# Kernel tuning notes

Hardware: AMD Instinct MI355X
Metric: run time of the kernel (lower is better)

The kernel has to match this reference:

```python
import jax, jax.numpy as jnp
import numpy as np

T, B, IN, HID, OUT = 100, 2048, 784, 100, 10
BETA = 0.9      # snn.Leaky(beta=0.9)
THRESH = 1.0    # snntorch default threshold
ALPHA = 2.0     # snntorch default ATan surrogate alpha

@jax.custom_vjp
def fire(x):
    # Heaviside spike with ATan surrogate gradient (snntorch default).
    return (x > 0).astype(x.dtype)

def _fire_fwd(x):
    return fire(x), x

def _fire_bwd(x, g):
    return (g * (ALPHA / 2) / (1 + (jnp.pi / 2 * ALPHA * x) ** 2),)

fire.defvjp(_fire_fwd, _fire_bwd)

def setup_inputs() -> dict:
    key = jax.random.key(0)
    k1, k2, k3 = jax.random.split(key, 3)
    x_seq = jax.random.normal(k1, (T, B, IN), dtype=jnp.float32)
    # nn.Linear weights are [out_features, in_features], bias=False
    w1 = jax.random.normal(k2, (HID, IN), dtype=jnp.float32) * (1.0 / np.sqrt(IN))
    w2 = jax.random.normal(k3, (OUT, HID), dtype=jnp.float32) * (1.0 / np.sqrt(HID))
    return {"x_seq": x_seq, "w1": w1, "w2": w2}

def _leaky_step(mem, cur):
    # snntorch Leaky, reset_mechanism='subtract':
    # reset = H(mem_prev - thresh) (detached); mem = beta*mem + input - reset*thresh; spk = fire(mem - thresh)
    reset = jax.lax.stop_gradient((mem > THRESH).astype(mem.dtype))
    mem = BETA * mem + cur - reset * THRESH
    spk = fire(mem - THRESH)
    return spk, mem

def reference(x_seq, w1, w2):
    batch = x_seq.shape[1]
    def step(carry, x_t):
        mem1, mem2 = carry
        spk1, mem1 = _leaky_step(mem1, x_t @ w1.T)      # [B,HID]
        spk2, mem2 = _leaky_step(mem2, spk1 @ w2.T)     # [B,OUT]
        return (mem1, mem2), spk2
    init = (jnp.zeros((batch, HID), x_seq.dtype),
            jnp.zeros((batch, OUT), x_seq.dtype))
    _, spk2_seq = jax.lax.scan(step, init, x_seq)
    return spk2_seq.sum(axis=0)  # spk2_sum: [B, OUT]
```

## Files before the change

### kernel.cpp

```cpp
#include <hip/hip_runtime.h>

#define T_STEPS 100
#define B_SZ    2048
#define IN_DIM  784
#define KPAD    800
#define HID_DIM 100
#define OUT_DIM 10
#define BN      112
#define BMR     64
#define KC      32
#define KSTEPS  25
#define WLP     113

typedef double f64x4 __attribute__((ext_vector_type(4)));
#define MFMA64(a, b, c) __builtin_amdgcn_mfma_f64_16x16x4f64((a), (b), (c), 0, 0, 0)

__global__ void pad_w1(const float* __restrict__ w1, float* __restrict__ w1p) {
  int i = blockIdx.x * 256 + threadIdx.x;
  if (i >= BN * KPAD) return;
  int r = i / KPAD, c = i % KPAD;
  w1p[i] = (r < HID_DIM && c < IN_DIM) ? w1[r * IN_DIM + c] : 0.0f;
}

__global__ __launch_bounds__(256, 4)
void snn_gemm1(const float* __restrict__ x,
               const float* __restrict__ w1p,
               double* __restrict__ cur)
{
  const int tid  = threadIdx.x;
  const int lane = tid & 63;
  const int wv   = tid >> 6;
  const int kg   = lane >> 4;
  const int il   = lane & 15;
  const long rowBase = (long)blockIdx.x * BMR;

  __shared__ float wls[2][KC][WLP];

  const int  wrow = tid >> 1;
  const int  wk0  = (tid & 1) * 16;
  const bool dow  = tid < 2 * BN;
  const float* wsrc = w1p + (long)wrow * KPAD + wk0;
  float4 wg0, wg1, wg2, wg3;

  auto WLOAD = [&](int s) {
    if (dow) {
      const float4* wp = reinterpret_cast<const float4*>(wsrc + s * KC);
      wg0 = wp[0]; wg1 = wp[1]; wg2 = wp[2]; wg3 = wp[3];
    }
  };
  auto WSTORE = [&](int buf) {
    if (dow) {
      float* b0 = &wls[buf][wk0][wrow];
      b0[0 * WLP] = wg0.x; b0[1 * WLP] = wg0.y; b0[2 * WLP]  = wg0.z; b0[3 * WLP]  = wg0.w;
      b0[4 * WLP] = wg1.x; b0[5 * WLP] = wg1.y; b0[6 * WLP]  = wg1.z; b0[7 * WLP]  = wg1.w;
      b0[8 * WLP] = wg2.x; b0[9 * WLP] = wg2.y; b0[10 * WLP] = wg2.z; b0[11 * WLP] = wg2.w;
      b0[12 * WLP] = wg3.x; b0[13 * WLP] = wg3.y; b0[14 * WLP] = wg3.z; b0[15 * WLP] = wg3.w;
    }
  };

  const float* xrp = x + (rowBase + wv * 16 + il) * (long)IN_DIM;
  float xcur[8], xnxt[8];
  auto XLOAD = [&](int s, float* d) {
    const int ks = s * KC + 8 * kg;
    if (s == KSTEPS - 1 && kg >= 2) {
#pragma unroll
      for (int j = 0; j < 8; ++j) d[j] = 0.0f;
    } else {
      *reinterpret_cast<float4*>(&d[0]) = *reinterpret_cast<const float4*>(xrp + ks);
      *reinterpret_cast<float4*>(&d[4]) = *reinterpret_cast<const float4*>(xrp + ks + 4);
    }
  };

  WLOAD(0); XLOAD(0, xcur);

  f64x4 z = {0.0, 0.0, 0.0, 0.0};
  const double eil = (double)il;
  const double d0 = (kg == 0) ? 1.0 : 0.0;
  const double d1 = (kg == 1) ? 1.0 : 0.0;
  const double d2 = (kg == 2) ? 1.0 : 0.0;
  const double d3 = (kg == 3) ? 1.0 : 0.0;
  const f64x4 Prow0 = MFMA64(eil, d0, z);
  const f64x4 Prow1 = MFMA64(eil, d1, z);
  const f64x4 Pcol0 = MFMA64(d0, eil, z);
  const f64x4 Pcol1 = MFMA64(d1, eil, z);
  const f64x4 Pv0   = MFMA64(d0, d0, z);
  const f64x4 Pv1   = MFMA64(d1, d1, z);
  const f64x4 Pv2   = MFMA64(d2, d2, z);
  const f64x4 Pv3   = MFMA64(d3, d3, z);

  bool okl = true;
  int rowof[4], colof[4];
#pragma unroll
  for (int r = 0; r < 4; ++r) {
    okl = okl && (Pv0[r] == 1.0) && (Pv1[r] == 1.0) && (Pv2[r] == 1.0) && (Pv3[r] == 1.0);
    okl = okl && (Prow0[r] == Prow1[r]) && (Pcol0[r] == Pcol1[r]);
    const int rr = (int)Prow0[r];
    const int cc = (int)Pcol0[r];
    okl = okl && ((double)rr == Prow0[r]) && (rr >= 0) && (rr < 16);
    okl = okl && ((double)cc == Pcol0[r]) && (cc >= 0) && (cc < 16);
    rowof[r] = rr; colof[r] = cc;
  }
  if (__all(okl ? 1 : 0) == 0) {
#pragma unroll
    for (int r = 0; r < 4; ++r) { rowof[r] = kg * 4 + r; colof[r] = il; }
  }

  f64x4 acc[7];
#pragma unroll
  for (int ht = 0; ht < 7; ++ht) acc[ht] = z;

  WSTORE(0); WLOAD(1);
  __syncthreads();

#pragma unroll 1
  for (int s = 0; s < KSTEPS; ++s) {
    const int buf = s & 1;
    if (s + 1 < KSTEPS) { WSTORE(buf ^ 1); XLOAD(s + 1, xnxt); }
    if (s + 2 < KSTEPS) WLOAD(s + 2);

#pragma unroll
    for (int m = 0; m < 8; ++m) {
      const double a0 = (double)xcur[m];
      double b[7];
#pragma unroll
      for (int ht = 0; ht < 7; ++ht)
        b[ht] = (double)wls[buf][8 * kg + m][ht * 16 + il];
#pragma unroll
      for (int ht = 0; ht < 7; ++ht)
        acc[ht] = MFMA64(a0, b[ht], acc[ht]);
    }
    __syncthreads();
#pragma unroll
    for (int j = 0; j < 8; ++j) xcur[j] = xnxt[j];
  }

  const long r0 = rowBase + wv * 16;
#pragma unroll
  for (int ht = 0; ht < 7; ++ht)
#pragma unroll
    for (int m = 0; m < 4; ++m)
      cur[(r0 + rowof[m]) * BN + ht * 16 + colof[m]] = acc[ht][m];
}

__global__ __launch_bounds__(256)
void snn_recur(const double* __restrict__ cur,
               const float* __restrict__ w2,
               double* __restrict__ mem1s, float* __restrict__ spk1s,
               double* __restrict__ mem2s, float* __restrict__ spk2s,
               float* __restrict__ outs,
               float* __restrict__ dout,
               int chunkT, int isFirst, int isLast)
{
  const int tid = threadIdx.x;
  const int b0  = blockIdx.x * 4;
  __shared__ float w2l[OUT_DIM * HID_DIM];
  __shared__ float spkl[4 * BN];

  if (tid < 250)
    reinterpret_cast<float4*>(w2l)[tid] = reinterpret_cast<const float4*>(w2)[tid];

  const bool pa = tid < 112;
  const int  sl = tid / 28, q4 = (tid % 28) * 4;
  const long aOff = (long)(b0 + sl) * BN + q4;
  double m1[4] = {0.0, 0.0, 0.0, 0.0};
  float4 s1 = make_float4(0.f, 0.f, 0.f, 0.f);
  if (pa && !isFirst) {
    const double2* mp = reinterpret_cast<const double2*>(mem1s + aOff);
    double2 a = mp[0], b = mp[1];
    m1[0] = a.x; m1[1] = a.y; m1[2] = b.x; m1[3] = b.y;
    s1 = *reinterpret_cast<const float4*>(spk1s + aOff);
  }

  const bool pb = tid < 80;
  const int  pp = tid >> 1, hf = tid & 1;
  const int  ss = pp / 10, oo = pp % 10;
  const long bOff = (long)b0 * OUT_DIM + pp;
  double m2 = 0.0;
  float s2 = 0.f, oacc = 0.f;
  if (pb && !isFirst && hf == 0) { m2 = mem2s[bOff]; s2 = spk2s[bOff]; oacc = outs[bOff]; }

  __syncthreads();

  double2 ca, cb;
  if (pa) {
    const double2* cp = reinterpret_cast<const double2*>(cur + (long)(b0 + sl) * BN + q4);
    ca = cp[0]; cb = cp[1];
  }

  for (int tt = 0; tt < chunkT; ++tt) {
    if (pa) {
      double cu[4] = {ca.x, ca.y, cb.x, cb.y};
      const int tn = (tt + 1 < chunkT) ? tt + 1 : tt;
      const double2* cp = reinterpret_cast<const double2*>(
          cur + ((long)tn * B_SZ + b0 + sl) * BN + q4);
      ca = cp[0]; cb = cp[1];

      float4 sp;
      float* spv = &sp.x;
      const float* s1v = &s1.x;
#pragma unroll
      for (int j = 0; j < 4; ++j) {
        double m = 0.9 * m1[j];
        m = m + cu[j];
        m = m - (double)s1v[j];
        spv[j] = (m > 1.0) ? 1.0f : 0.0f;
        m1[j] = m;
      }
      s1 = sp;
      *reinterpret_cast<float4*>(&spkl[sl * BN + q4]) = sp;
    }
    __syncthreads();
    if (pb) {
      const float* sr = &spkl[ss * BN] + hf * 50;
      const float* wr = &w2l[oo * HID_DIM] + hf * 50;
      double a0 = 0.0, a1 = 0.0;
#pragma unroll
      for (int h = 0; h < 50; h += 2) {
        a0 = fma((double)sr[h],     (double)wr[h],     a0);
        a1 = fma((double)sr[h + 1], (double)wr[h + 1], a1);
      }
      double a = a0 + a1;
      a = a + __shfl_xor(a, 1);
      if (hf == 0) {
        double m = 0.9 * m2;
        m = m + a;
        m = m - (double)s2;
        const float sp = (m > 1.0) ? 1.0f : 0.0f;
        m2 = m; s2 = sp; oacc += sp;
      }
    }
    __syncthreads();
  }

  if (pa) {
    double2* mp = reinterpret_cast<double2*>(mem1s + aOff);
    mp[0] = make_double2(m1[0], m1[1]);
    mp[1] = make_double2(m1[2], m1[3]);
    *reinterpret_cast<float4*>(spk1s + aOff) = s1;
  }
  if (pb && hf == 0) {
    mem2s[bOff] = m2; spk2s[bOff] = s2; outs[bOff] = oacc;
    if (isLast) dout[bOff] = oacc;
  }
}

extern "C" void kernel_launch(void* const* d_in, const int* in_sizes, int n_in,
                              void* d_out, int out_size, void* d_ws, size_t ws_size,
                              hipStream_t stream) {
  const float* x  = (const float*)d_in[0];
  const float* w1 = (const float*)d_in[1];
  const float* w2 = (const float*)d_in[2];
  float* out = (float*)d_out;

  char* ws = (char*)d_ws;
  float*  w1p   = (float*) (ws);
  double* mem1s = (double*)(ws +  358400);
  float*  spk1s = (float*) (ws + 2193408);
  double* mem2s = (double*)(ws + 3110912);
  float*  spk2s = (float*) (ws + 3274752);
  float*  outs  = (float*) (ws + 3356672);
  double* cur   = (double*)(ws + 3438592);

  pad_w1<<<dim3((BN * KPAD + 255) / 256), dim3(256), 0, stream>>>(w1, w1p);

  const size_t perT = (size_t)B_SZ * BN * 8;
  size_t curCap = ws_size > (size_t)3438592 ? ws_size - 3438592 : 0;
  int Tc = (int)(curCap / perT);
  if (Tc > T_STEPS) Tc = T_STEPS;
  if (Tc < 1) Tc = 1;

  for (int t0 = 0; t0 < T_STEPS; t0 += Tc) {
    const int ct = (T_STEPS - t0 < Tc) ? (T_STEPS - t0) : Tc;
    snn_gemm1<<<dim3(ct * (B_SZ / BMR)), dim3(256), 0, stream>>>(
        x + (size_t)t0 * B_SZ * IN_DIM, w1p, cur);
    snn_recur<<<dim3(B_SZ / 4), dim3(256), 0, stream>>>(
        cur, w2, mem1s, spk1s, mem2s, spk2s, outs, out,
        ct, (t0 == 0) ? 1 : 0, (t0 + ct >= T_STEPS) ? 1 : 0);
  }
}
```

Baseline: 771.5 us.

## Load W1 directly from global into registers, dropping LDS staging and pad kernel

The GEMM1 kernel no longer stages padded W1 tiles through double-buffered shared memory with barriers. Each lane now loads its W1 fragments straight from the unpadded w1 into registers via float4 loads, clamping rows and K offsets so the padding is never read, and the pad_w1 launch is removed. This drops LDS traffic, syncthreads and one kernel launch, in exchange for redundant global/L2 loads of W1 across waves and higher register pressure, which is why launch bounds drop from 4 to 3 blocks.

```diff
diff --git a/kernel.cpp b/kernel.cpp
--- a/kernel.cpp
+++ b/kernel.cpp
@@ -3,28 +3,19 @@
 #define T_STEPS 100
 #define B_SZ    2048
 #define IN_DIM  784
-#define KPAD    800
 #define HID_DIM 100
 #define OUT_DIM 10
 #define BN      112
 #define BMR     64
 #define KC      32
 #define KSTEPS  25
-#define WLP     113
 
 typedef double f64x4 __attribute__((ext_vector_type(4)));
 #define MFMA64(a, b, c) __builtin_amdgcn_mfma_f64_16x16x4f64((a), (b), (c), 0, 0, 0)
 
-__global__ void pad_w1(const float* __restrict__ w1, float* __restrict__ w1p) {
-  int i = blockIdx.x * 256 + threadIdx.x;
-  if (i >= BN * KPAD) return;
-  int r = i / KPAD, c = i % KPAD;
-  w1p[i] = (r < HID_DIM && c < IN_DIM) ? w1[r * IN_DIM + c] : 0.0f;
-}
-
-__global__ __launch_bounds__(256, 4)
+__global__ __launch_bounds__(256, 3)
 void snn_gemm1(const float* __restrict__ x,
-               const float* __restrict__ w1p,
+               const float* __restrict__ w1,
                double* __restrict__ cur)
 {
   const int tid  = threadIdx.x;
@@ -34,44 +25,30 @@
   const int il   = lane & 15;
   const long rowBase = (long)blockIdx.x * BMR;
 
-  __shared__ float wls[2][KC][WLP];
-
-  const int  wrow = tid >> 1;
-  const int  wk0  = (tid & 1) * 16;
-  const bool dow  = tid < 2 * BN;
-  const float* wsrc = w1p + (long)wrow * KPAD + wk0;
-  float4 wg0, wg1, wg2, wg3;
-
-  auto WLOAD = [&](int s) {
-    if (dow) {
-      const float4* wp = reinterpret_cast<const float4*>(wsrc + s * KC);
-      wg0 = wp[0]; wg1 = wp[1]; wg2 = wp[2]; wg3 = wp[3];
-    }
-  };
-  auto WSTORE = [&](int buf) {
-    if (dow) {
-      float* b0 = &wls[buf][wk0][wrow];
-      b0[0 * WLP] = wg0.x; b0[1 * WLP] = wg0.y; b0[2 * WLP]  = wg0.z; b0[3 * WLP]  = wg0.w;
-      b0[4 * WLP] = wg1.x; b0[5 * WLP] = wg1.y; b0[6 * WLP]  = wg1.z; b0[7 * WLP]  = wg1.w;
-      b0[8 * WLP] = wg2.x; b0[9 * WLP] = wg2.y; b0[10 * WLP] = wg2.z; b0[11 * WLP] = wg2.w;
-      b0[12 * WLP] = wg3.x; b0[13 * WLP] = wg3.y; b0[14 * WLP] = wg3.z; b0[15 * WLP] = wg3.w;
-    }
-  };
-
+  int rowoff[7];
+#pragma unroll
+  for (int ht = 0; ht < 7; ++ht) {
+    int r = ht * 16 + il;
+    if (r > HID_DIM - 1) r = HID_DIM - 1;
+    rowoff[ht] = r * IN_DIM;
+  }
+
+  const int kg8 = kg * 8;
   const float* xrp = x + (rowBase + wv * 16 + il) * (long)IN_DIM;
+
   float xcur[8], xnxt[8];
   auto XLOAD = [&](int s, float* d) {
-    const int ks = s * KC + 8 * kg;
     if (s == KSTEPS - 1 && kg >= 2) {
 #pragma unroll
       for (int j = 0; j < 8; ++j) d[j] = 0.0f;
     } else {
-      *reinterpret_cast<float4*>(&d[0]) = *reinterpret_cast<const float4*>(xrp + ks);
-      *reinterpret_cast<float4*>(&d[4]) = *reinterpret_cast<const float4*>(xrp + ks + 4);
+      const float* p = xrp + s * KC + kg8;
+      *reinterpret_cast<float4*>(&d[0]) = *reinterpret_cast<const float4*>(p);
+      *reinterpret_cast<float4*>(&d[4]) = *reinterpret_cast<const float4*>(p + 4);
     }
   };
 
-  WLOAD(0); XLOAD(0, xcur);
+  XLOAD(0, xcur);
 
   f64x4 z = {0.0, 0.0, 0.0, 0.0};
   const double eil = (double)il;
@@ -109,27 +86,29 @@
 #pragma unroll
   for (int ht = 0; ht < 7; ++ht) acc[ht] = z;
 
-  WSTORE(0); WLOAD(1);
-  __syncthreads();
-
 #pragma unroll 1
   for (int s = 0; s < KSTEPS; ++s) {
-    const int buf = s & 1;
-    if (s + 1 < KSTEPS) { WSTORE(buf ^ 1); XLOAD(s + 1, xnxt); }
-    if (s + 2 < KSTEPS) WLOAD(s + 2);
+    if (s + 1 < KSTEPS) XLOAD(s + 1, xnxt);
+
+    int k0 = s * KC + kg8;
+    if (s == KSTEPS - 1 && kg >= 2) k0 = kg8;
+    float4 wa[7], wb[7];
+#pragma unroll
+    for (int ht = 0; ht < 7; ++ht) {
+      const float* p = w1 + rowoff[ht] + k0;
+      wa[ht] = *reinterpret_cast<const float4*>(p);
+      wb[ht] = *reinterpret_cast<const float4*>(p + 4);
+    }
 
 #pragma unroll
     for (int m = 0; m < 8; ++m) {
       const double a0 = (double)xcur[m];
-      double b[7];
-#pragma unroll
-      for (int ht = 0; ht < 7; ++ht)
-        b[ht] = (double)wls[buf][8 * kg + m][ht * 16 + il];
-#pragma unroll
-      for (int ht = 0; ht < 7; ++ht)
-        acc[ht] = MFMA64(a0, b[ht], acc[ht]);
-    }
-    __syncthreads();
+#pragma unroll
+      for (int ht = 0; ht < 7; ++ht) {
+        const float wf = (m < 4) ? (&wa[ht].x)[m] : (&wb[ht].x)[m - 4];
+        acc[ht] = MFMA64(a0, (double)wf, acc[ht]);
+      }
+    }
 #pragma unroll
     for (int j = 0; j < 8; ++j) xcur[j] = xnxt[j];
   }
@@ -253,18 +232,15 @@
   float* out = (float*)d_out;
 
   char* ws = (char*)d_ws;
-  float*  w1p   = (float*) (ws);
-  double* mem1s = (double*)(ws +  358400);
-  float*  spk1s = (float*) (ws + 2193408);
-  double* mem2s = (double*)(ws + 3110912);
-  float*  spk2s = (float*) (ws + 3274752);
-  float*  outs  = (float*) (ws + 3356672);
-  double* cur   = (double*)(ws + 3438592);
-
-  pad_w1<<<dim3((BN * KPAD + 255) / 256), dim3(256), 0, stream>>>(w1, w1p);
+  double* mem1s = (double*)(ws);
+  float*  spk1s = (float*) (ws + 1835008);
+  double* mem2s = (double*)(ws + 2752512);
+  float*  spk2s = (float*) (ws + 2916352);
+  float*  outs  = (float*) (ws + 2998272);
+  double* cur   = (double*)(ws + 3080192);
 
   const size_t perT = (size_t)B_SZ * BN * 8;
-  size_t curCap = ws_size > (size_t)3438592 ? ws_size - 3438592 : 0;
+  size_t curCap = ws_size > (size_t)3080192 ? ws_size - 3080192 : 0;
   int Tc = (int)(curCap / perT);
   if (Tc > T_STEPS) Tc = T_STEPS;
   if (Tc < 1) Tc = 1;
@@ -272,7 +248,7 @@
   for (int t0 = 0; t0 < T_STEPS; t0 += Tc) {
     const int ct = (T_STEPS - t0 < Tc) ? (T_STEPS - t0) : Tc;
     snn_gemm1<<<dim3(ct * (B_SZ / BMR)), dim3(256), 0, stream>>>(
-        x + (size_t)t0 * B_SZ * IN_DIM, w1p, cur);
+        x + (size_t)t0 * B_SZ * IN_DIM, w1, cur);
     snn_recur<<<dim3(B_SZ / 4), dim3(256), 0, stream>>>(
         cur, w2, mem1s, spk1s, mem2s, spk2s, outs, out,
         ct, (t0 == 0) ? 1 : 0, (t0 + ct >= T_STEPS) ? 1 : 0);
```

New measurement: 835.5 us. 1.08x slower.

## Double row tile per wave in FP64 MFMA GEMM1 and transpose W1 LDS layout

Applied to the files above, without the earlier changes.

Each wave now computes two 16-row tiles (BMR 64->128), so every W1 value read from LDS feeds two MFMAs and the LDS traffic per FLOP is halved. The shared W1 tile is stored row-major by hidden unit with a padded K stride, which lets the store and the per-thread reads use float4 vector accesses in place of scalar strided ones. In exchange each thread holds twice as many accumulators, launch bounds drop to 2 blocks per CU, and there are half as many blocks in the grid.

```diff
diff --git a/kernel.cpp b/kernel.cpp
--- a/kernel.cpp
+++ b/kernel.cpp
@@ -7,10 +7,10 @@
 #define HID_DIM 100
 #define OUT_DIM 10
 #define BN      112
-#define BMR     64
+#define BMR     128
 #define KC      32
 #define KSTEPS  25
-#define WLP     113
+#define WLP     36
 
 typedef double f64x4 __attribute__((ext_vector_type(4)));
 #define MFMA64(a, b, c) __builtin_amdgcn_mfma_f64_16x16x4f64((a), (b), (c), 0, 0, 0)
@@ -22,7 +22,7 @@
   w1p[i] = (r < HID_DIM && c < IN_DIM) ? w1[r * IN_DIM + c] : 0.0f;
 }
 
-__global__ __launch_bounds__(256, 4)
+__global__ __launch_bounds__(256, 2)
 void snn_gemm1(const float* __restrict__ x,
                const float* __restrict__ w1p,
                double* __restrict__ cur)
@@ -32,14 +32,15 @@
   const int wv   = tid >> 6;
   const int kg   = lane >> 4;
   const int il   = lane & 15;
+  const int kg8  = kg * 8;
   const long rowBase = (long)blockIdx.x * BMR;
 
-  __shared__ float wls[2][KC][WLP];
+  __shared__ float wls[2][BN][WLP];
 
   const int  wrow = tid >> 1;
-  const int  wk0  = (tid & 1) * 16;
+  const int  wh0  = (tid & 1) * 16;
   const bool dow  = tid < 2 * BN;
-  const float* wsrc = w1p + (long)wrow * KPAD + wk0;
+  const float* wsrc = w1p + (long)wrow * KPAD + wh0;
   float4 wg0, wg1, wg2, wg3;
 
   auto WLOAD = [&](int s) {
@@ -50,24 +51,25 @@
   };
   auto WSTORE = [&](int buf) {
     if (dow) {
-      float* b0 = &wls[buf][wk0][wrow];
-      b0[0 * WLP] = wg0.x; b0[1 * WLP] = wg0.y; b0[2 * WLP]  = wg0.z; b0[3 * WLP]  = wg0.w;
-      b0[4 * WLP] = wg1.x; b0[5 * WLP] = wg1.y; b0[6 * WLP]  = wg1.z; b0[7 * WLP]  = wg1.w;
-      b0[8 * WLP] = wg2.x; b0[9 * WLP] = wg2.y; b0[10 * WLP] = wg2.z; b0[11 * WLP] = wg2.w;
-      b0[12 * WLP] = wg3.x; b0[13 * WLP] = wg3.y; b0[14 * WLP] = wg3.z; b0[15 * WLP] = wg3.w;
+      float4* b0 = reinterpret_cast<float4*>(&wls[buf][wrow][wh0]);
+      b0[0] = wg0; b0[1] = wg1; b0[2] = wg2; b0[3] = wg3;
     }
   };
 
-  const float* xrp = x + (rowBase + wv * 16 + il) * (long)IN_DIM;
-  float xcur[8], xnxt[8];
-  auto XLOAD = [&](int s, float* d) {
-    const int ks = s * KC + 8 * kg;
+  const float* xr0 = x + (rowBase + wv * 32 + il) * (long)IN_DIM;
+  const float* xr1 = xr0 + 16 * (long)IN_DIM;
+  float xcur[2][8], xnxt[2][8];
+  auto XLOAD = [&](int s, float (*d)[8]) {
     if (s == KSTEPS - 1 && kg >= 2) {
 #pragma unroll
-      for (int j = 0; j < 8; ++j) d[j] = 0.0f;
+      for (int j = 0; j < 8; ++j) { d[0][j] = 0.0f; d[1][j] = 0.0f; }
     } else {
-      *reinterpret_cast<float4*>(&d[0]) = *reinterpret_cast<const float4*>(xrp + ks);
-      *reinterpret_cast<float4*>(&d[4]) = *reinterpret_cast<const float4*>(xrp + ks + 4);
+      const float* p0 = xr0 + s * KC + kg8;
+      const float* p1 = xr1 + s * KC + kg8;
+      *reinterpret_cast<float4*>(&d[0][0]) = *reinterpret_cast<const float4*>(p0);
+      *reinterpret_cast<float4*>(&d[0][4]) = *reinterpret_cast<const float4*>(p0 + 4);
+      *reinterpret_cast<float4*>(&d[1][0]) = *reinterpret_cast<const float4*>(p1);
+      *reinterpret_cast<float4*>(&d[1][4]) = *reinterpret_cast<const float4*>(p1 + 4);
     }
   };
 
@@ -105,9 +107,11 @@
     for (int r = 0; r < 4; ++r) { rowof[r] = kg * 4 + r; colof[r] = il; }
   }
 
-  f64x4 acc[7];
-#pragma unroll
-  for (int ht = 0; ht < 7; ++ht) acc[ht] = z;
+  f64x4 acc[2][7];
+#pragma unroll
+  for (int rt = 0; rt < 2; ++rt)
+#pragma unroll
+    for (int ht = 0; ht < 7; ++ht) acc[rt][ht] = z;
 
   WSTORE(0); WLOAD(1);
   __syncthreads();
@@ -118,28 +122,49 @@
     if (s + 1 < KSTEPS) { WSTORE(buf ^ 1); XLOAD(s + 1, xnxt); }
     if (s + 2 < KSTEPS) WLOAD(s + 2);
 
-#pragma unroll
-    for (int m = 0; m < 8; ++m) {
-      const double a0 = (double)xcur[m];
-      double b[7];
-#pragma unroll
-      for (int ht = 0; ht < 7; ++ht)
-        b[ht] = (double)wls[buf][8 * kg + m][ht * 16 + il];
-#pragma unroll
-      for (int ht = 0; ht < 7; ++ht)
-        acc[ht] = MFMA64(a0, b[ht], acc[ht]);
+    double dx0[8], dx1[8];
+#pragma unroll
+    for (int j = 0; j < 8; ++j) {
+      dx0[j] = (double)xcur[0][j];
+      dx1[j] = (double)xcur[1][j];
+    }
+
+#pragma unroll
+    for (int ht = 0; ht < 7; ++ht) {
+      const float* wrp = &wls[buf][ht * 16 + il][kg8];
+      const float4 f0 = *reinterpret_cast<const float4*>(wrp);
+      const float4 f1 = *reinterpret_cast<const float4*>(wrp + 4);
+      acc[0][ht] = MFMA64(dx0[0], (double)f0.x, acc[0][ht]);
+      acc[1][ht] = MFMA64(dx1[0], (double)f0.x, acc[1][ht]);
+      acc[0][ht] = MFMA64(dx0[1], (double)f0.y, acc[0][ht]);
+      acc[1][ht] = MFMA64(dx1[1], (double)f0.y, acc[1][ht]);
+      acc[0][ht] = MFMA64(dx0[2], (double)f0.z, acc[0][ht]);
+      acc[1][ht] = MFMA64(dx1[2], (double)f0.z, acc[1][ht]);
+      acc[0][ht] = MFMA64(dx0[3], (double)f0.w, acc[0][ht]);
+      acc[1][ht] = MFMA64(dx1[3], (double)f0.w, acc[1][ht]);
+      acc[0][ht] = MFMA64(dx0[4], (double)f1.x, acc[0][ht]);
+      acc[1][ht] = MFMA64(dx1[4], (double)f1.x, acc[1][ht]);
+      acc[0][ht] = MFMA64(dx0[5], (double)f1.y, acc[0][ht]);
+      acc[1][ht] = MFMA64(dx1[5], (double)f1.y, acc[1][ht]);
+      acc[0][ht] = MFMA64(dx0[6], (double)f1.z, acc[0][ht]);
+      acc[1][ht] = MFMA64(dx1[6], (double)f1.z, acc[1][ht]);
+      acc[0][ht] = MFMA64(dx0[7], (double)f1.w, acc[0][ht]);
+      acc[1][ht] = MFMA64(dx1[7], (double)f1.w, acc[1][ht]);
     }
     __syncthreads();
 #pragma unroll
-    for (int j = 0; j < 8; ++j) xcur[j] = xnxt[j];
-  }
-
-  const long r0 = rowBase + wv * 16;
-#pragma unroll
-  for (int ht = 0; ht < 7; ++ht)
-#pragma unroll
-    for (int m = 0; m < 4; ++m)
-      cur[(r0 + rowof[m]) * BN + ht * 16 + colof[m]] = acc[ht][m];
+    for (int j = 0; j < 8; ++j) { xcur[0][j] = xnxt[0][j]; xcur[1][j] = xnxt[1][j]; }
+  }
+
+#pragma unroll
+  for (int rt = 0; rt < 2; ++rt) {
+    const long r0 = rowBase + wv * 32 + rt * 16;
+#pragma unroll
+    for (int ht = 0; ht < 7; ++ht)
+#pragma unroll
+      for (int m = 0; m < 4; ++m)
+        cur[(r0 + rowof[m]) * BN + ht * 16 + colof[m]] = acc[rt][ht][m];
+  }
 }
 
 __global__ __launch_bounds__(256)
```

Result: slower. 818.9 us (+6.1%).
